# Kernel optimization log

Measured on AMD Instinct MI355X. Metric: run time of the kernel, lower is better.

## Reference

```python
import jax, jax.numpy as jnp
import numpy as np

NUM_USERS = 100000
NUM_ITEMS = 50000
LATENT_DIM = 64
N_EDGES = 600000
BATCH = 4096
N_LAYERS = 4  # K=4, time_split=4, euler -> 4 unit propagation steps


def setup_inputs() -> dict:
    key = jax.random.key(0)
    k1, k2, k3, k4, k5, k6 = jax.random.split(key, 6)
    return {
        "users": jax.random.randint(k1, (BATCH,), 0, NUM_USERS),
        "items": jax.random.randint(k2, (BATCH,), 0, NUM_ITEMS),
        "edge_u": jax.random.randint(k3, (N_EDGES,), 0, NUM_USERS),
        "edge_i": jax.random.randint(k4, (N_EDGES,), 0, NUM_ITEMS),
        "user_emb": 0.1 * jax.random.normal(k5, (NUM_USERS, LATENT_DIM), dtype=jnp.float32),
        "item_emb": 0.1 * jax.random.normal(k6, (NUM_ITEMS, LATENT_DIM), dtype=jnp.float32),
    }


def reference(users, items, edge_u, edge_i, user_emb, item_emb):
    num_users = user_emb.shape[0]
    num_items = item_emb.shape[0]
    N = num_users + num_items

    # symmetric bipartite adjacency as directed edge list
    src = jnp.concatenate([edge_u, edge_i + num_users])
    dst = jnp.concatenate([edge_i + num_users, edge_u])

    # D^{-1/2} A D^{-1/2} edge weights (LightGCN normalization)
    deg = jax.ops.segment_sum(jnp.ones_like(src, dtype=jnp.float32), src, num_segments=N)
    inv_sqrt = jnp.where(deg > 0, jax.lax.rsqrt(jnp.maximum(deg, 1.0)), 0.0)
    w = inv_sqrt[src] * inv_sqrt[dst]  # [2E]

    def spmm(x):  # A_hat @ x via gather-scale-scatter
        return jax.ops.segment_sum(w[:, None] * x[src], dst, num_segments=N)

    x0 = jnp.concatenate([user_emb, item_emb], axis=0)  # [N, d]
    # ODE euler step x + A x, then residual subtraction -> stored emb = A^k x0
    embs = [x0]
    e = x0
    for _ in range(N_LAYERS):
        e = spmm(e)
        embs.append(e)
    light_out = jnp.mean(jnp.stack(embs, axis=1), axis=1)  # [N, d]

    all_users = light_out[:num_users]
    all_items = light_out[num_users:]
    users_emb = all_users[users]
    items_emb = all_items[items]
    gamma = jnp.sum(users_emb * items_emb, axis=1)  # [B]
    return gamma
```

## Files before the change

kernel.cpp:

```cpp
#include <hip/hip_runtime.h>

#define WAVE 64
#define BROWS 256
#define NBKT_MAX 1024
#define CMAX 4
#define SRCMASK 0x3FFFF
#define EPB 2048
#define ENTCAP 4096


__device__ __forceinline__ unsigned short f2bf(float f) {
    unsigned u = __float_as_uint(f);
    u += 0x7FFF + ((u >> 16) & 1);
    return (unsigned short)(u >> 16);
}
__device__ __forceinline__ float bf2f(unsigned short v) {
    return __uint_as_float((unsigned)v << 16);
}
__device__ __forceinline__ void addbf8(float* a, uint4 v) {
    a[0] += __uint_as_float(v.x << 16);
    a[1] += __uint_as_float(v.x & 0xFFFF0000u);
    a[2] += __uint_as_float(v.y << 16);
    a[3] += __uint_as_float(v.y & 0xFFFF0000u);
    a[4] += __uint_as_float(v.z << 16);
    a[5] += __uint_as_float(v.z & 0xFFFF0000u);
    a[6] += __uint_as_float(v.w << 16);
    a[7] += __uint_as_float(v.w & 0xFFFF0000u);
}

__global__ void k_hist(const int* __restrict__ eu, const int* __restrict__ ei,
                       int nE, int nU, int nBkt, int nJg, int* __restrict__ cntBB) {
    __shared__ int h4[4 * NBKT_MAX];
    for (int i = threadIdx.x; i < 4 * nBkt; i += 256) h4[i] = 0;
    __syncthreads();
    int* hw = h4 + (threadIdx.x >> 6) * nBkt;
    const int4* eu4 = (const int4*)eu;
    const int4* ei4 = (const int4*)ei;
    for (int pass = 0; pass < 2; pass++) {
        int i4 = blockIdx.x * 512 + pass * 256 + threadIdx.x;
        int e0 = i4 * 4;
        if (e0 + 3 < nE) {
            int4 u = eu4[i4];
            int4 v = ei4[i4];
            atomicAdd(&hw[u.x >> 8], 1); atomicAdd(&hw[(nU + v.x) >> 8], 1);
            atomicAdd(&hw[u.y >> 8], 1); atomicAdd(&hw[(nU + v.y) >> 8], 1);
            atomicAdd(&hw[u.z >> 8], 1); atomicAdd(&hw[(nU + v.z) >> 8], 1);
            atomicAdd(&hw[u.w >> 8], 1); atomicAdd(&hw[(nU + v.w) >> 8], 1);
        } else if (e0 < nE) {
            for (int e = e0; e < nE; e++) {
                atomicAdd(&hw[eu[e] >> 8], 1);
                atomicAdd(&hw[(nU + ei[e]) >> 8], 1);
            }
        }
    }
    __syncthreads();
    int j = (blockIdx.x & 7) * nJg + (blockIdx.x >> 3);
    int* dst = cntBB + (size_t)j * nBkt;
    for (int i = threadIdx.x; i < nBkt; i += 256)
        dst[i] = h4[i] + h4[nBkt + i] + h4[2 * nBkt + i] + h4[3 * nBkt + i];
}

__global__ void k_scanBkt(const int* __restrict__ cntBB, int* __restrict__ baseBB,
                          int* __restrict__ bktTot, int nBkt, int nJ) {
    __shared__ int s[256];
    int b = blockIdx.x, t = threadIdx.x;
    int C = (nJ + 255) / 256;
    int vals[CMAX];
    int sum = 0;
    for (int k = 0; k < CMAX; k++) {
        if (k >= C) break;
        int j = t * C + k;
        int v = (j < nJ) ? cntBB[(size_t)j * nBkt + b] : 0;
        vals[k] = v; sum += v;
    }
    s[t] = sum;
    __syncthreads();
    for (int o = 1; o < 256; o <<= 1) {
        int x = (t >= o) ? s[t - o] : 0;
        __syncthreads();
        s[t] += x;
        __syncthreads();
    }
    int run = s[t] - sum;
    for (int k = 0; k < CMAX; k++) {
        if (k >= C) break;
        int j = t * C + k;
        if (j < nJ) { baseBB[(size_t)b * nJ + j] = run; run += vals[k]; }
    }
    if (t == 0) bktTot[b] = s[255];
}

__global__ void k_scanTot(const int* __restrict__ bktTot, int* __restrict__ bktBase,
                          int* __restrict__ row_ptr, int nBkt, int N, int total) {
    __shared__ int s[1024];
    int t = threadIdx.x;
    int v = (t < nBkt) ? bktTot[t] : 0;
    s[t] = v;
    __syncthreads();
    for (int o = 1; o < 1024; o <<= 1) {
        int x = (t >= o) ? s[t - o] : 0;
        __syncthreads();
        s[t] += x;
        __syncthreads();
    }
    if (t < nBkt) bktBase[t] = s[t] - v;
    if (t == 0) { bktBase[nBkt] = total; row_ptr[N] = total; }
}

__global__ void k_bin(const int* __restrict__ eu, const int* __restrict__ ei,
                      int nE, int nU, int nBkt, int nJ, int nJg,
                      const int* __restrict__ baseBB, const int* __restrict__ bktBase,
                      int* __restrict__ bins) {
    __shared__ int ent[2 * EPB];
    __shared__ unsigned short ebkt[2 * EPB];
    __shared__ int h2[2 * NBKT_MAX];
    __shared__ int lcur[NBKT_MAX];
    __shared__ int dlt[NBKT_MAX];
    __shared__ int sp[256];
    int t = threadIdx.x;
    int j = (blockIdx.x & 7) * nJg + (blockIdx.x >> 3);
    const bool fullBlk = ((size_t)(blockIdx.x + 1) * EPB <= (size_t)nE);

    if (!fullBlk) {
        for (int i = t; i < nBkt; i += 256)
            lcur[i] = bktBase[i] + baseBB[(size_t)i * nJ + j];
        __syncthreads();
        for (int e = blockIdx.x * EPB + t; e < nE; e += 256) {
            int u = eu[e];
            int v = nU + ei[e];
            int p1 = atomicAdd(&lcur[u >> 8], 1);
            int p2 = atomicAdd(&lcur[v >> 8], 1);
            bins[p1] = ((u & 255) << 18) | v;
            bins[p2] = ((v & 255) << 18) | u;
        }
        return;
    }

    for (int i = t; i < nBkt; i += 256) { h2[i] = 0; h2[NBKT_MAX + i] = 0; }
    __syncthreads();
    int myb[16], mye[16];
    int* hs = h2 + (t >> 7) * NBKT_MAX;
    {
        const int4* eu4 = (const int4*)eu;
        const int4* ei4 = (const int4*)ei;
        #pragma unroll
        for (int pass = 0; pass < 2; pass++) {
            int i4 = blockIdx.x * 512 + pass * 256 + t;
            int4 uu = eu4[i4];
            int4 vv = ei4[i4];
            #pragma unroll
            for (int k = 0; k < 4; k++) {
                int u = (k == 0) ? uu.x : (k == 1) ? uu.y : (k == 2) ? uu.z : uu.w;
                int i2 = (k == 0) ? vv.x : (k == 1) ? vv.y : (k == 2) ? vv.z : vv.w;
                int v = nU + i2;
                int idx = pass * 8 + k * 2;
                myb[idx]     = u >> 8; mye[idx]     = ((u & 255) << 18) | v;
                myb[idx + 1] = v >> 8; mye[idx + 1] = ((v & 255) << 18) | u;
            }
        }
    }
    #pragma unroll
    for (int k = 0; k < 16; k++) atomicAdd(&hs[myb[k]], 1);
    __syncthreads();
    int C = (nBkt + 255) / 256;
    int vals[4];
    int sum = 0;
    for (int k = 0; k < 4; k++) {
        if (k >= C) break;
        int b = t * C + k;
        int v = (b < nBkt) ? (h2[b] + h2[NBKT_MAX + b]) : 0;
        vals[k] = v; sum += v;
    }
    sp[t] = sum;
    __syncthreads();
    for (int o = 1; o < 256; o <<= 1) {
        int x = (t >= o) ? sp[t - o] : 0;
        __syncthreads();
        sp[t] += x;
        __syncthreads();
    }
    int run = sp[t] - sum;
    for (int k = 0; k < 4; k++) {
        if (k >= C) break;
        int b = t * C + k;
        if (b < nBkt) {
            lcur[b] = run;
            int g = bktBase[b] + baseBB[(size_t)b * nJ + j];
            dlt[b] = g - run;
            run += vals[k];
        }
    }
    __syncthreads();
    int n4 = sp[255];
    #pragma unroll
    for (int k = 0; k < 16; k++) {
        int p = atomicAdd(&lcur[myb[k]], 1);
        ent[p] = mye[k];
        ebkt[p] = (unsigned short)myb[k];
    }
    __syncthreads();
    for (int i = t; i < n4; i += 256)
        bins[dlt[ebkt[i]] + i] = ent[i];
}

__global__ void k_csrz(const int* __restrict__ bins, const int* __restrict__ bktBase,
                       int N, int nU,
                       const float* __restrict__ ue, const float* __restrict__ ie,
                       int* __restrict__ row_ptr, int* __restrict__ col,
                       unsigned short* __restrict__ z0) {
    __shared__ int ent[ENTCAP];
    __shared__ int h4[4 * BROWS];
    __shared__ int sc[BROWS];
    __shared__ int cur4[4 * BROWS];
    __shared__ float sInv[BROWS];
    int b = blockIdx.x, t = threadIdx.x, w = t >> 6;
    int base = bktBase[b];
    int n = bktBase[b + 1] - base;
    h4[t] = 0; h4[256 + t] = 0; h4[512 + t] = 0; h4[768 + t] = 0;
    __syncthreads();
    int* hw = h4 + w * BROWS;
    for (int i = t; i < n; i += 256) {
        int p = bins[base + i];
        if (i < ENTCAP) ent[i] = p;
        atomicAdd(&hw[p >> 18], 1);
    }
    __syncthreads();
    int v = h4[t] + h4[256 + t] + h4[512 + t] + h4[768 + t];
    sc[t] = v;
    __syncthreads();
    for (int o = 1; o < 256; o <<= 1) {
        int x = (t >= o) ? sc[t - o] : 0;
        __syncthreads();
        sc[t] += x;
        __syncthreads();
    }
    int excl = sc[t] - v;
    int row = b * BROWS + t;
    if (row < N) row_ptr[row] = base + excl;
    sInv[t] = (v > 0) ? (1.0f / sqrtf((float)v)) : 0.0f;
    cur4[t]       = excl;
    cur4[256 + t] = excl + h4[t];
    cur4[512 + t] = excl + h4[t] + h4[256 + t];
    cur4[768 + t] = excl + h4[t] + h4[256 + t] + h4[512 + t];
    __syncthreads();
    int rf = t & 15, rg = t >> 4;
    for (int pass = 0; pass < 16; pass++) {
        int r = pass * 16 + rg;
        int rr = b * BROWS + r;
        if (rr < N) {
            const float4* src = (rr < nU)
                ? ((const float4*)ue) + (size_t)rr * 16
                : ((const float4*)ie) + (size_t)(rr - nU) * 16;
            float4 val = src[rf];
            float scl = sInv[r];
            ushort4 o;
            o.x = f2bf(val.x * scl);
            o.y = f2bf(val.y * scl);
            o.z = f2bf(val.z * scl);
            o.w = f2bf(val.w * scl);
            ((ushort4*)z0)[(size_t)rr * 16 + rf] = o;
        }
    }
    int* cw = cur4 + w * BROWS;
    for (int i = t; i < n; i += 256) {
        int p = (i < ENTCAP) ? ent[i] : bins[base + i];
        int pos = base + atomicAdd(&cw[p >> 18], 1);
        col[pos] = p & SRCMASK;
    }
}

__global__ void k_spmm(const int* __restrict__ row_ptr, const int* __restrict__ col,
                       const unsigned short* __restrict__ x,
                       unsigned short* __restrict__ y, int N, int nBlkMain,
                       const int* __restrict__ users, const int* __restrict__ items,
                       int B, int nU,
                       const float* __restrict__ ue, const float* __restrict__ ie,
                       float* __restrict__ acc, int mode) {
    int t = threadIdx.x;
    if ((int)blockIdx.x < nBlkMain) {
        int grp = t >> 3, f = t & 7;
        int row = blockIdx.x * 32 + grp;
        if (row >= N) return;
        const uint4* x8 = (const uint4*)x;
        int s = row_ptr[row], e = row_ptr[row + 1];
        float a0[8] = {0,0,0,0,0,0,0,0};
        float a1[8] = {0,0,0,0,0,0,0,0};
        float a2[8] = {0,0,0,0,0,0,0,0};
        float a3[8] = {0,0,0,0,0,0,0,0};
        for (int j = s; j < e; j += 8) {
            #pragma unroll
            for (int k = 0; k < 8; k++) {
                int jj = j + k;
                bool ok = jj < e;
                int c = col[ok ? jj : (e - 1)];
                uint4 v = x8[(size_t)c * 8 + f];
                if (!ok) { v.x = 0; v.y = 0; v.z = 0; v.w = 0; }
                if ((k & 3) == 0) addbf8(a0, v);
                else if ((k & 3) == 1) addbf8(a1, v);
                else if ((k & 3) == 2) addbf8(a2, v);
                else addbf8(a3, v);
            }
        }
        float rdeg = (e > s) ? (1.0f / (float)(e - s)) : 0.0f;
        uint4 o;
        float s0, s1;
        s0 = (a0[0]+a1[0]+a2[0]+a3[0]) * rdeg; s1 = (a0[1]+a1[1]+a2[1]+a3[1]) * rdeg;
        o.x = (unsigned)f2bf(s0) | ((unsigned)f2bf(s1) << 16);
        s0 = (a0[2]+a1[2]+a2[2]+a3[2]) * rdeg; s1 = (a0[3]+a1[3]+a2[3]+a3[3]) * rdeg;
        o.y = (unsigned)f2bf(s0) | ((unsigned)f2bf(s1) << 16);
        s0 = (a0[4]+a1[4]+a2[4]+a3[4]) * rdeg; s1 = (a0[5]+a1[5]+a2[5]+a3[5]) * rdeg;
        o.z = (unsigned)f2bf(s0) | ((unsigned)f2bf(s1) << 16);
        s0 = (a0[6]+a1[6]+a2[6]+a3[6]) * rdeg; s1 = (a0[7]+a1[7]+a2[7]+a3[7]) * rdeg;
        o.w = (unsigned)f2bf(s0) | ((unsigned)f2bf(s1) << 16);
        ((uint4*)y)[(size_t)row * 8 + f] = o;
    } else {
        int grp = t >> 4, f4 = t & 15;
        int b = (blockIdx.x - nBlkMain) * 16 + grp;
        if (b >= 2 * B) return;
        const ushort4* x4 = (const ushort4*)x;
        float4 c;
        if (mode == 0) {
            const float4* x0 = (b < B)
                ? ((const float4*)ue) + (size_t)users[b] * 16
                : ((const float4*)ie) + (size_t)items[b - B] * 16;
            c = x0[f4];
        } else {
            int row = (b < B) ? users[b] : (nU + items[b - B]);
            int deg = row_ptr[row + 1] - row_ptr[row];
            float f = sqrtf((float)deg);
            ushort4 v = x4[(size_t)row * 16 + f4];
            c = ((const float4*)acc)[(size_t)b * 16 + f4];
            c.x += f * bf2f(v.x); c.y += f * bf2f(v.y);
            c.z += f * bf2f(v.z); c.w += f * bf2f(v.w);
        }
        ((float4*)acc)[(size_t)b * 16 + f4] = c;
    }
}

__global__ void k_tail34(const int* __restrict__ row_ptr, const int* __restrict__ col,
                         const unsigned short* __restrict__ z3,
                         const int* __restrict__ users, const int* __restrict__ items,
                         int B, int nU, float* __restrict__ acc) {
    int t = threadIdx.x, grp = t >> 3, f = t & 7;
    int b = blockIdx.x * 32 + grp;
    if (b >= 2 * B) return;
    int row = (b < B) ? users[b] : (nU + items[b - B]);
    int s = row_ptr[row], e = row_ptr[row + 1];
    const uint4* x8 = (const uint4*)z3;
    float4 cA = ((const float4*)acc)[(size_t)b * 16 + 2 * f];
    float4 cB = ((const float4*)acc)[(size_t)b * 16 + 2 * f + 1];
    if (e > s) {
        float fq = sqrtf((float)(e - s));
        float a0[8] = {0,0,0,0,0,0,0,0};
        float a1[8] = {0,0,0,0,0,0,0,0};
        int j = s;
        for (; j + 1 < e; j += 2) {
            uint4 v0 = x8[(size_t)col[j] * 8 + f];
            uint4 v1 = x8[(size_t)col[j + 1] * 8 + f];
            addbf8(a0, v0); addbf8(a1, v1);
        }
        if (j < e) {
            uint4 v0 = x8[(size_t)col[j] * 8 + f];
            addbf8(a0, v0);
        }
        uint4 vs = x8[(size_t)row * 8 + f];
        float self[8] = {0,0,0,0,0,0,0,0};
        addbf8(self, vs);
        float scale = fq / (float)(e - s);
        cA.x += fq * self[0] + scale * (a0[0] + a1[0]);
        cA.y += fq * self[1] + scale * (a0[1] + a1[1]);
        cA.z += fq * self[2] + scale * (a0[2] + a1[2]);
        cA.w += fq * self[3] + scale * (a0[3] + a1[3]);
        cB.x += fq * self[4] + scale * (a0[4] + a1[4]);
        cB.y += fq * self[5] + scale * (a0[5] + a1[5]);
        cB.z += fq * self[6] + scale * (a0[6] + a1[6]);
        cB.w += fq * self[7] + scale * (a0[7] + a1[7]);
    }
    ((float4*)acc)[(size_t)b * 16 + 2 * f]     = cA;
    ((float4*)acc)[(size_t)b * 16 + 2 * f + 1] = cB;
}

__global__ void k_dot(const float* __restrict__ acc, int B, float* __restrict__ out) {
    int b = blockIdx.x * (blockDim.x >> 6) + (threadIdx.x >> 6);
    int lane = threadIdx.x & 63;
    if (b >= B) return;
    float p = acc[(size_t)b * 64 + lane] * acc[(size_t)(b + B) * 64 + lane];
    #pragma unroll
    for (int o = 32; o > 0; o >>= 1) p += __shfl_down(p, o, WAVE);
    if (lane == 0) out[b] = p * (1.0f / 25.0f);
}

extern "C" void kernel_launch(void* const* d_in, const int* in_sizes, int n_in,
                              void* d_out, int out_size, void* d_ws, size_t ws_size,
                              hipStream_t stream) {
    const int*   users = (const int*)d_in[0];
    const int*   items = (const int*)d_in[1];
    const int*   eu    = (const int*)d_in[2];
    const int*   ei    = (const int*)d_in[3];
    const float* ue    = (const float*)d_in[4];
    const float* ie    = (const float*)d_in[5];
    float* out = (float*)d_out;

    const int D  = 64;
    const int B  = in_sizes[0];
    const int nE = in_sizes[2];
    const int nU = in_sizes[4] / D;
    const int nI = in_sizes[5] / D;
    const int N  = nU + nI;
    const int nBkt = (N + BROWS - 1) / BROWS;
    const int total = 2 * nE;

    const int nBlkB = (nE + EPB - 1) / EPB;
    const int nJg   = (nBlkB + 7) / 8;
    const int nJ    = 8 * nJg;

    char* p = (char*)d_ws;
    auto alloc = [&](size_t bytes) -> void* {
        void* r = (void*)p;
        p += (bytes + 255) & ~(size_t)255;
        return r;
    };
    int*   cntBB   = (int*)  alloc((size_t)nJ * nBkt * 4);
    int*   baseBB  = (int*)  alloc((size_t)nBkt * nJ * 4);
    int*   bktTot  = (int*)  alloc((size_t)nBkt * 4);
    int*   bktBase = (int*)  alloc((size_t)(nBkt + 1) * 4);
    int*   bins    = (int*)  alloc((size_t)total * 4);
    int*   col     = (int*)  alloc((size_t)total * 4);
    int*   row_ptr = (int*)  alloc((size_t)(N + 1) * 4);
    unsigned short* za = (unsigned short*)alloc((size_t)N * D * 2);
    unsigned short* zb = (unsigned short*)alloc((size_t)N * D * 2);
    float* acc     = (float*)alloc((size_t)2 * B * D * 4);

    k_hist<<<nJ, 256, 0, stream>>>(eu, ei, nE, nU, nBkt, nJg, cntBB);
    k_scanBkt<<<nBkt, 256, 0, stream>>>(cntBB, baseBB, bktTot, nBkt, nJ);
    k_scanTot<<<1, 1024, 0, stream>>>(bktTot, bktBase, row_ptr, nBkt, N, total);
    k_bin<<<nJ, 256, 0, stream>>>(eu, ei, nE, nU, nBkt, nJ, nJg, baseBB, bktBase, bins);
    k_csrz<<<nBkt, BROWS, 0, stream>>>(bins, bktBase, N, nU, ue, ie, row_ptr, col, za);

    const int nBlkMain = (N + 31) / 32;
    const int nBlkTail = (2 * B + 15) / 16;
    unsigned short* zin = za;
    unsigned short* zout = zb;
    for (int l = 0; l < 3; l++) {
        k_spmm<<<nBlkMain + nBlkTail, 256, 0, stream>>>(
            row_ptr, col, zin, zout, N, nBlkMain,
            users, items, B, nU, ue, ie, acc, (l == 0) ? 0 : 1);
        unsigned short* t = zin; zin = zout; zout = t;
    }

    const int nBlkT34 = (2 * B + 31) / 32;
    k_tail34<<<nBlkT34, 256, 0, stream>>>(row_ptr, col, zin, users, items, B, nU, acc);
    k_dot<<<(B + 3) / 4, 256, 0, stream>>>(acc, B, out);
}
```

Baseline: 210.8 us.

## Fuse CSR build pipeline into one cooperative kernel with grid syncs

Replaces the five separate CSR construction kernels (histogram, per-bucket scan, total scan, binning, CSR+z0 init) with a single cooperative kernel of 512 blocks that steps through the phases separated by grid.sync. The chunk size drops to 1024 edges, and the layer-0 acc initialization moves into the build kernel's otherwise idle blocks, so the first spmm launch no longer needs tail blocks. The goal is to remove launch gaps and kernel-boundary drains between the small phases. In exchange, grid-wide barriers are added, the grid is fixed at 512 blocks that loop over the work, and there are more per-chunk partial counts to scan.

```diff
diff --git a/kernel.cpp b/kernel.cpp
--- a/kernel.cpp
+++ b/kernel.cpp
@@ -1,12 +1,14 @@
 #include <hip/hip_runtime.h>
+#include <hip/hip_cooperative_groups.h>
+
+namespace cg = cooperative_groups;
 
 #define WAVE 64
 #define BROWS 256
-#define NBKT_MAX 1024
-#define CMAX 4
 #define SRCMASK 0x3FFFF
-#define EPB 2048
+#define EPC 1024
 #define ENTCAP 4096
+#define GRID_BUILD 512
 
 
 __device__ __forceinline__ unsigned short f2bf(float f) {
@@ -28,244 +30,267 @@
     a[7] += __uint_as_float(v.w & 0xFFFF0000u);
 }
 
-__global__ void k_hist(const int* __restrict__ eu, const int* __restrict__ ei,
-                       int nE, int nU, int nBkt, int nJg, int* __restrict__ cntBB) {
-    __shared__ int h4[4 * NBKT_MAX];
-    for (int i = threadIdx.x; i < 4 * nBkt; i += 256) h4[i] = 0;
-    __syncthreads();
-    int* hw = h4 + (threadIdx.x >> 6) * nBkt;
-    const int4* eu4 = (const int4*)eu;
-    const int4* ei4 = (const int4*)ei;
-    for (int pass = 0; pass < 2; pass++) {
-        int i4 = blockIdx.x * 512 + pass * 256 + threadIdx.x;
-        int e0 = i4 * 4;
-        if (e0 + 3 < nE) {
-            int4 u = eu4[i4];
-            int4 v = ei4[i4];
-            atomicAdd(&hw[u.x >> 8], 1); atomicAdd(&hw[(nU + v.x) >> 8], 1);
-            atomicAdd(&hw[u.y >> 8], 1); atomicAdd(&hw[(nU + v.y) >> 8], 1);
-            atomicAdd(&hw[u.z >> 8], 1); atomicAdd(&hw[(nU + v.z) >> 8], 1);
-            atomicAdd(&hw[u.w >> 8], 1); atomicAdd(&hw[(nU + v.w) >> 8], 1);
-        } else if (e0 < nE) {
-            for (int e = e0; e < nE; e++) {
-                atomicAdd(&hw[eu[e] >> 8], 1);
-                atomicAdd(&hw[(nU + ei[e]) >> 8], 1);
-            }
-        }
-    }
-    __syncthreads();
-    int j = (blockIdx.x & 7) * nJg + (blockIdx.x >> 3);
-    int* dst = cntBB + (size_t)j * nBkt;
-    for (int i = threadIdx.x; i < nBkt; i += 256)
-        dst[i] = h4[i] + h4[nBkt + i] + h4[2 * nBkt + i] + h4[3 * nBkt + i];
-}
-
-__global__ void k_scanBkt(const int* __restrict__ cntBB, int* __restrict__ baseBB,
-                          int* __restrict__ bktTot, int nBkt, int nJ) {
-    __shared__ int s[256];
-    int b = blockIdx.x, t = threadIdx.x;
-    int C = (nJ + 255) / 256;
-    int vals[CMAX];
-    int sum = 0;
-    for (int k = 0; k < CMAX; k++) {
-        if (k >= C) break;
-        int j = t * C + k;
-        int v = (j < nJ) ? cntBB[(size_t)j * nBkt + b] : 0;
-        vals[k] = v; sum += v;
-    }
-    s[t] = sum;
-    __syncthreads();
-    for (int o = 1; o < 256; o <<= 1) {
-        int x = (t >= o) ? s[t - o] : 0;
+__global__ void k_build(const int* __restrict__ eu, const int* __restrict__ ei,
+                        int nE, int nU, int nBkt, int nChunk,
+                        int* __restrict__ cntBB, int* __restrict__ baseBB,
+                        int* __restrict__ bktTot, int* __restrict__ bktBase,
+                        int* __restrict__ bins, int* __restrict__ row_ptr,
+                        int* __restrict__ col, unsigned short* __restrict__ z0,
+                        const float* __restrict__ ue, const float* __restrict__ ie,
+                        const int* __restrict__ users, const int* __restrict__ items,
+                        int B, float* __restrict__ acc, int N, int total) {
+    cg::grid_group grid = cg::this_grid();
+    __shared__ __align__(16) char smem[30720];
+    int t = threadIdx.x;
+
+    {
+        int* h4 = (int*)smem;
+        for (int c = blockIdx.x; c < nChunk; c += gridDim.x) {
+            for (int i = t; i < 4 * nBkt; i += 256) h4[i] = 0;
+            __syncthreads();
+            int* hw = h4 + (t >> 6) * nBkt;
+            if ((c + 1) * EPC <= nE) {
+                int i4 = c * 256 + t;
+                int4 u = ((const int4*)eu)[i4];
+                int4 v = ((const int4*)ei)[i4];
+                atomicAdd(&hw[u.x >> 8], 1); atomicAdd(&hw[(nU + v.x) >> 8], 1);
+                atomicAdd(&hw[u.y >> 8], 1); atomicAdd(&hw[(nU + v.y) >> 8], 1);
+                atomicAdd(&hw[u.z >> 8], 1); atomicAdd(&hw[(nU + v.z) >> 8], 1);
+                atomicAdd(&hw[u.w >> 8], 1); atomicAdd(&hw[(nU + v.w) >> 8], 1);
+            } else {
+                for (int e = c * EPC + t; e < nE; e += 256) {
+                    atomicAdd(&hw[eu[e] >> 8], 1);
+                    atomicAdd(&hw[(nU + ei[e]) >> 8], 1);
+                }
+            }
+            __syncthreads();
+            int* dst = cntBB + (size_t)c * nBkt;
+            for (int i = t; i < nBkt; i += 256)
+                dst[i] = h4[i] + h4[nBkt + i] + h4[2 * nBkt + i] + h4[3 * nBkt + i];
+            __syncthreads();
+        }
+    }
+    grid.sync();
+
+    {
+        int* sp = (int*)smem;
+        int C = (nChunk + 255) / 256;
+        for (int b = blockIdx.x; b < nBkt; b += gridDim.x) {
+            int vals[4];
+            int sum = 0;
+            for (int k = 0; k < 4; k++) {
+                if (k >= C) break;
+                int j = t * C + k;
+                int v = (j < nChunk) ? cntBB[(size_t)j * nBkt + b] : 0;
+                vals[k] = v; sum += v;
+            }
+            sp[t] = sum;
+            __syncthreads();
+            for (int o = 1; o < 256; o <<= 1) {
+                int x = (t >= o) ? sp[t - o] : 0;
+                __syncthreads();
+                sp[t] += x;
+                __syncthreads();
+            }
+            int run = sp[t] - sum;
+            for (int k = 0; k < 4; k++) {
+                if (k >= C) break;
+                int j = t * C + k;
+                if (j < nChunk) { baseBB[(size_t)b * nChunk + j] = run; run += vals[k]; }
+            }
+            if (t == 0) bktTot[b] = sp[255];
+            __syncthreads();
+        }
+    }
+    grid.sync();
+
+    if (blockIdx.x == 0) {
+        int* sp = (int*)smem;
+        int C = (nBkt + 255) / 256;
+        int vals[4];
+        int sum = 0;
+        for (int k = 0; k < 4; k++) {
+            if (k >= C) break;
+            int i = t * C + k;
+            int v = (i < nBkt) ? bktTot[i] : 0;
+            vals[k] = v; sum += v;
+        }
+        sp[t] = sum;
         __syncthreads();
-        s[t] += x;
-        __syncthreads();
-    }
-    int run = s[t] - sum;
-    for (int k = 0; k < CMAX; k++) {
-        if (k >= C) break;
-        int j = t * C + k;
-        if (j < nJ) { baseBB[(size_t)b * nJ + j] = run; run += vals[k]; }
-    }
-    if (t == 0) bktTot[b] = s[255];
-}
-
-__global__ void k_scanTot(const int* __restrict__ bktTot, int* __restrict__ bktBase,
-                          int* __restrict__ row_ptr, int nBkt, int N, int total) {
-    __shared__ int s[1024];
-    int t = threadIdx.x;
-    int v = (t < nBkt) ? bktTot[t] : 0;
-    s[t] = v;
-    __syncthreads();
-    for (int o = 1; o < 1024; o <<= 1) {
-        int x = (t >= o) ? s[t - o] : 0;
-        __syncthreads();
-        s[t] += x;
-        __syncthreads();
-    }
-    if (t < nBkt) bktBase[t] = s[t] - v;
-    if (t == 0) { bktBase[nBkt] = total; row_ptr[N] = total; }
-}
-
-__global__ void k_bin(const int* __restrict__ eu, const int* __restrict__ ei,
-                      int nE, int nU, int nBkt, int nJ, int nJg,
-                      const int* __restrict__ baseBB, const int* __restrict__ bktBase,
-                      int* __restrict__ bins) {
-    __shared__ int ent[2 * EPB];
-    __shared__ unsigned short ebkt[2 * EPB];
-    __shared__ int h2[2 * NBKT_MAX];
-    __shared__ int lcur[NBKT_MAX];
-    __shared__ int dlt[NBKT_MAX];
-    __shared__ int sp[256];
-    int t = threadIdx.x;
-    int j = (blockIdx.x & 7) * nJg + (blockIdx.x >> 3);
-    const bool fullBlk = ((size_t)(blockIdx.x + 1) * EPB <= (size_t)nE);
-
-    if (!fullBlk) {
-        for (int i = t; i < nBkt; i += 256)
-            lcur[i] = bktBase[i] + baseBB[(size_t)i * nJ + j];
-        __syncthreads();
-        for (int e = blockIdx.x * EPB + t; e < nE; e += 256) {
-            int u = eu[e];
-            int v = nU + ei[e];
-            int p1 = atomicAdd(&lcur[u >> 8], 1);
-            int p2 = atomicAdd(&lcur[v >> 8], 1);
-            bins[p1] = ((u & 255) << 18) | v;
-            bins[p2] = ((v & 255) << 18) | u;
-        }
-        return;
-    }
-
-    for (int i = t; i < nBkt; i += 256) { h2[i] = 0; h2[NBKT_MAX + i] = 0; }
-    __syncthreads();
-    int myb[16], mye[16];
-    int* hs = h2 + (t >> 7) * NBKT_MAX;
+        for (int o = 1; o < 256; o <<= 1) {
+            int x = (t >= o) ? sp[t - o] : 0;
+            __syncthreads();
+            sp[t] += x;
+            __syncthreads();
+        }
+        int run = sp[t] - sum;
+        for (int k = 0; k < 4; k++) {
+            if (k >= C) break;
+            int i = t * C + k;
+            if (i < nBkt) { bktBase[i] = run; run += vals[k]; }
+        }
+        if (t == 0) { bktBase[nBkt] = total; row_ptr[N] = total; }
+    } else {
+        for (int idx = (blockIdx.x - 1) * 256 + t; idx < 2 * B * 16;
+             idx += (gridDim.x - 1) * 256) {
+            int b = idx >> 4, f4 = idx & 15;
+            const float4* x0 = (b < B)
+                ? ((const float4*)ue) + (size_t)users[b] * 16
+                : ((const float4*)ie) + (size_t)items[b - B] * 16;
+            ((float4*)acc)[(size_t)b * 16 + f4] = x0[f4];
+        }
+    }
+    grid.sync();
+
     {
-        const int4* eu4 = (const int4*)eu;
-        const int4* ei4 = (const int4*)ei;
-        #pragma unroll
-        for (int pass = 0; pass < 2; pass++) {
-            int i4 = blockIdx.x * 512 + pass * 256 + t;
-            int4 uu = eu4[i4];
-            int4 vv = ei4[i4];
-            #pragma unroll
-            for (int k = 0; k < 4; k++) {
-                int u = (k == 0) ? uu.x : (k == 1) ? uu.y : (k == 2) ? uu.z : uu.w;
-                int i2 = (k == 0) ? vv.x : (k == 1) ? vv.y : (k == 2) ? vv.z : vv.w;
-                int v = nU + i2;
-                int idx = pass * 8 + k * 2;
-                myb[idx]     = u >> 8; mye[idx]     = ((u & 255) << 18) | v;
-                myb[idx + 1] = v >> 8; mye[idx + 1] = ((v & 255) << 18) | u;
-            }
-        }
-    }
-    #pragma unroll
-    for (int k = 0; k < 16; k++) atomicAdd(&hs[myb[k]], 1);
-    __syncthreads();
-    int C = (nBkt + 255) / 256;
-    int vals[4];
-    int sum = 0;
-    for (int k = 0; k < 4; k++) {
-        if (k >= C) break;
-        int b = t * C + k;
-        int v = (b < nBkt) ? (h2[b] + h2[NBKT_MAX + b]) : 0;
-        vals[k] = v; sum += v;
-    }
-    sp[t] = sum;
-    __syncthreads();
-    for (int o = 1; o < 256; o <<= 1) {
-        int x = (t >= o) ? sp[t - o] : 0;
-        __syncthreads();
-        sp[t] += x;
-        __syncthreads();
-    }
-    int run = sp[t] - sum;
-    for (int k = 0; k < 4; k++) {
-        if (k >= C) break;
-        int b = t * C + k;
-        if (b < nBkt) {
-            lcur[b] = run;
-            int g = bktBase[b] + baseBB[(size_t)b * nJ + j];
-            dlt[b] = g - run;
-            run += vals[k];
-        }
-    }
-    __syncthreads();
-    int n4 = sp[255];
-    #pragma unroll
-    for (int k = 0; k < 16; k++) {
-        int p = atomicAdd(&lcur[myb[k]], 1);
-        ent[p] = mye[k];
-        ebkt[p] = (unsigned short)myb[k];
-    }
-    __syncthreads();
-    for (int i = t; i < n4; i += 256)
-        bins[dlt[ebkt[i]] + i] = ent[i];
-}
-
-__global__ void k_csrz(const int* __restrict__ bins, const int* __restrict__ bktBase,
-                       int N, int nU,
-                       const float* __restrict__ ue, const float* __restrict__ ie,
-                       int* __restrict__ row_ptr, int* __restrict__ col,
-                       unsigned short* __restrict__ z0) {
-    __shared__ int ent[ENTCAP];
-    __shared__ int h4[4 * BROWS];
-    __shared__ int sc[BROWS];
-    __shared__ int cur4[4 * BROWS];
-    __shared__ float sInv[BROWS];
-    int b = blockIdx.x, t = threadIdx.x, w = t >> 6;
-    int base = bktBase[b];
-    int n = bktBase[b + 1] - base;
-    h4[t] = 0; h4[256 + t] = 0; h4[512 + t] = 0; h4[768 + t] = 0;
-    __syncthreads();
-    int* hw = h4 + w * BROWS;
-    for (int i = t; i < n; i += 256) {
-        int p = bins[base + i];
-        if (i < ENTCAP) ent[i] = p;
-        atomicAdd(&hw[p >> 18], 1);
-    }
-    __syncthreads();
-    int v = h4[t] + h4[256 + t] + h4[512 + t] + h4[768 + t];
-    sc[t] = v;
-    __syncthreads();
-    for (int o = 1; o < 256; o <<= 1) {
-        int x = (t >= o) ? sc[t - o] : 0;
-        __syncthreads();
-        sc[t] += x;
-        __syncthreads();
-    }
-    int excl = sc[t] - v;
-    int row = b * BROWS + t;
-    if (row < N) row_ptr[row] = base + excl;
-    sInv[t] = (v > 0) ? (1.0f / sqrtf((float)v)) : 0.0f;
-    cur4[t]       = excl;
-    cur4[256 + t] = excl + h4[t];
-    cur4[512 + t] = excl + h4[t] + h4[256 + t];
-    cur4[768 + t] = excl + h4[t] + h4[256 + t] + h4[512 + t];
-    __syncthreads();
-    int rf = t & 15, rg = t >> 4;
-    for (int pass = 0; pass < 16; pass++) {
-        int r = pass * 16 + rg;
-        int rr = b * BROWS + r;
-        if (rr < N) {
-            const float4* src = (rr < nU)
-                ? ((const float4*)ue) + (size_t)rr * 16
-                : ((const float4*)ie) + (size_t)(rr - nU) * 16;
-            float4 val = src[rf];
-            float scl = sInv[r];
-            ushort4 o;
-            o.x = f2bf(val.x * scl);
-            o.y = f2bf(val.y * scl);
-            o.z = f2bf(val.z * scl);
-            o.w = f2bf(val.w * scl);
-            ((ushort4*)z0)[(size_t)rr * 16 + rf] = o;
-        }
-    }
-    int* cw = cur4 + w * BROWS;
-    for (int i = t; i < n; i += 256) {
-        int p = (i < ENTCAP) ? ent[i] : bins[base + i];
-        int pos = base + atomicAdd(&cw[p >> 18], 1);
-        col[pos] = p & SRCMASK;
+        int* ent            = (int*)smem;
+        unsigned short* ebk = (unsigned short*)(smem + 8192);
+        int* h2             = (int*)(smem + 12288);
+        int* lcur           = (int*)(smem + 20480);
+        int* dlt            = (int*)(smem + 24576);
+        int* sp             = (int*)(smem + 28672);
+        for (int c = blockIdx.x; c < nChunk; c += gridDim.x) {
+            if ((c + 1) * EPC <= nE) {
+                for (int i = t; i < 2 * nBkt; i += 256) h2[i] = 0;
+                __syncthreads();
+                int myb[8], mye[8];
+                {
+                    int i4 = c * 256 + t;
+                    int4 uu = ((const int4*)eu)[i4];
+                    int4 vv = ((const int4*)ei)[i4];
+                    #pragma unroll
+                    for (int k = 0; k < 4; k++) {
+                        int u  = (k == 0) ? uu.x : (k == 1) ? uu.y : (k == 2) ? uu.z : uu.w;
+                        int i2 = (k == 0) ? vv.x : (k == 1) ? vv.y : (k == 2) ? vv.z : vv.w;
+                        int v = nU + i2;
+                        myb[2 * k]     = u >> 8; mye[2 * k]     = ((u & 255) << 18) | v;
+                        myb[2 * k + 1] = v >> 8; mye[2 * k + 1] = ((v & 255) << 18) | u;
+                    }
+                }
+                int* hs = h2 + (t >> 7) * nBkt;
+                #pragma unroll
+                for (int k = 0; k < 8; k++) atomicAdd(&hs[myb[k]], 1);
+                __syncthreads();
+                int C = (nBkt + 255) / 256;
+                int vals[4];
+                int sum = 0;
+                for (int k = 0; k < 4; k++) {
+                    if (k >= C) break;
+                    int b = t * C + k;
+                    int v = (b < nBkt) ? (h2[b] + h2[nBkt + b]) : 0;
+                    vals[k] = v; sum += v;
+                }
+                sp[t] = sum;
+                __syncthreads();
+                for (int o = 1; o < 256; o <<= 1) {
+                    int x = (t >= o) ? sp[t - o] : 0;
+                    __syncthreads();
+                    sp[t] += x;
+                    __syncthreads();
+                }
+                int run = sp[t] - sum;
+                for (int k = 0; k < 4; k++) {
+                    if (k >= C) break;
+                    int b = t * C + k;
+                    if (b < nBkt) {
+                        lcur[b] = run;
+                        dlt[b] = bktBase[b] + baseBB[(size_t)b * nChunk + c] - run;
+                        run += vals[k];
+                    }
+                }
+                __syncthreads();
+                #pragma unroll
+                for (int k = 0; k < 8; k++) {
+                    int p = atomicAdd(&lcur[myb[k]], 1);
+                    ent[p] = mye[k];
+                    ebk[p] = (unsigned short)myb[k];
+                }
+                __syncthreads();
+                int n4 = sp[255];
+                for (int i = t; i < n4; i += 256)
+                    bins[dlt[ebk[i]] + i] = ent[i];
+                __syncthreads();
+            } else {
+                for (int i = t; i < nBkt; i += 256)
+                    lcur[i] = bktBase[i] + baseBB[(size_t)i * nChunk + c];
+                __syncthreads();
+                for (int e = c * EPC + t; e < nE; e += 256) {
+                    int u = eu[e];
+                    int v = nU + ei[e];
+                    int p1 = atomicAdd(&lcur[u >> 8], 1);
+                    int p2 = atomicAdd(&lcur[v >> 8], 1);
+                    bins[p1] = ((u & 255) << 18) | v;
+                    bins[p2] = ((v & 255) << 18) | u;
+                }
+                __syncthreads();
+            }
+        }
+    }
+    grid.sync();
+
+    {
+        int* ent    = (int*)smem;
+        int* h4     = (int*)(smem + 16384);
+        int* cur4   = (int*)(smem + 20480);
+        int* sc     = (int*)(smem + 24576);
+        float* sInv = (float*)(smem + 25600);
+        int w = t >> 6;
+        for (int b = blockIdx.x; b < nBkt; b += gridDim.x) {
+            int base = bktBase[b];
+            int n = bktBase[b + 1] - base;
+            h4[t] = 0; h4[256 + t] = 0; h4[512 + t] = 0; h4[768 + t] = 0;
+            __syncthreads();
+            int* hw = h4 + w * BROWS;
+            for (int i = t; i < n; i += 256) {
+                int p = bins[base + i];
+                if (i < ENTCAP) ent[i] = p;
+                atomicAdd(&hw[p >> 18], 1);
+            }
+            __syncthreads();
+            int v = h4[t] + h4[256 + t] + h4[512 + t] + h4[768 + t];
+            sc[t] = v;
+            __syncthreads();
+            for (int o = 1; o < 256; o <<= 1) {
+                int x = (t >= o) ? sc[t - o] : 0;
+                __syncthreads();
+                sc[t] += x;
+                __syncthreads();
+            }
+            int excl = sc[t] - v;
+            int row = b * BROWS + t;
+            if (row < N) row_ptr[row] = base + excl;
+            sInv[t] = (v > 0) ? (1.0f / sqrtf((float)v)) : 0.0f;
+            cur4[t]       = excl;
+            cur4[256 + t] = excl + h4[t];
+            cur4[512 + t] = excl + h4[t] + h4[256 + t];
+            cur4[768 + t] = excl + h4[t] + h4[256 + t] + h4[512 + t];
+            __syncthreads();
+            int rf = t & 15, rg = t >> 4;
+            for (int pass = 0; pass < 16; pass++) {
+                int r = pass * 16 + rg;
+                int rr = b * BROWS + r;
+                if (rr < N) {
+                    const float4* src = (rr < nU)
+                        ? ((const float4*)ue) + (size_t)rr * 16
+                        : ((const float4*)ie) + (size_t)(rr - nU) * 16;
+                    float4 val = src[rf];
+                    float scl = sInv[r];
+                    ushort4 o;
+                    o.x = f2bf(val.x * scl);
+                    o.y = f2bf(val.y * scl);
+                    o.z = f2bf(val.z * scl);
+                    o.w = f2bf(val.w * scl);
+                    ((ushort4*)z0)[(size_t)rr * 16 + rf] = o;
+                }
+            }
+            int* cw = cur4 + w * BROWS;
+            for (int i = t; i < n; i += 256) {
+                int p = (i < ENTCAP) ? ent[i] : bins[base + i];
+                int pos = base + atomicAdd(&cw[p >> 18], 1);
+                col[pos] = p & SRCMASK;
+            }
+            __syncthreads();
+        }
     }
 }
 
@@ -273,9 +298,7 @@
                        const unsigned short* __restrict__ x,
                        unsigned short* __restrict__ y, int N, int nBlkMain,
                        const int* __restrict__ users, const int* __restrict__ items,
-                       int B, int nU,
-                       const float* __restrict__ ue, const float* __restrict__ ie,
-                       float* __restrict__ acc, int mode) {
+                       int B, int nU, float* __restrict__ acc, int mode) {
     int t = threadIdx.x;
     if ((int)blockIdx.x < nBlkMain) {
         int grp = t >> 3, f = t & 7;
@@ -314,25 +337,18 @@
         o.w = (unsigned)f2bf(s0) | ((unsigned)f2bf(s1) << 16);
         ((uint4*)y)[(size_t)row * 8 + f] = o;
     } else {
+        if (mode == 0) return;
         int grp = t >> 4, f4 = t & 15;
         int b = (blockIdx.x - nBlkMain) * 16 + grp;
         if (b >= 2 * B) return;
         const ushort4* x4 = (const ushort4*)x;
-        float4 c;
-        if (mode == 0) {
-            const float4* x0 = (b < B)
-                ? ((const float4*)ue) + (size_t)users[b] * 16
-                : ((const float4*)ie) + (size_t)items[b - B] * 16;
-            c = x0[f4];
-        } else {
-            int row = (b < B) ? users[b] : (nU + items[b - B]);
-            int deg = row_ptr[row + 1] - row_ptr[row];
-            float f = sqrtf((float)deg);
-            ushort4 v = x4[(size_t)row * 16 + f4];
-            c = ((const float4*)acc)[(size_t)b * 16 + f4];
-            c.x += f * bf2f(v.x); c.y += f * bf2f(v.y);
-            c.z += f * bf2f(v.z); c.w += f * bf2f(v.w);
-        }
+        int row = (b < B) ? users[b] : (nU + items[b - B]);
+        int deg = row_ptr[row + 1] - row_ptr[row];
+        float f = sqrtf((float)deg);
+        ushort4 v = x4[(size_t)row * 16 + f4];
+        float4 c = ((const float4*)acc)[(size_t)b * 16 + f4];
+        c.x += f * bf2f(v.x); c.y += f * bf2f(v.y);
+        c.z += f * bf2f(v.z); c.w += f * bf2f(v.w);
         ((float4*)acc)[(size_t)b * 16 + f4] = c;
     }
 }
@@ -402,17 +418,14 @@
     float* out = (float*)d_out;
 
     const int D  = 64;
-    const int B  = in_sizes[0];
-    const int nE = in_sizes[2];
-    const int nU = in_sizes[4] / D;
+    int B  = in_sizes[0];
+    int nE = in_sizes[2];
+    int nU = in_sizes[4] / D;
     const int nI = in_sizes[5] / D;
-    const int N  = nU + nI;
-    const int nBkt = (N + BROWS - 1) / BROWS;
-    const int total = 2 * nE;
-
-    const int nBlkB = (nE + EPB - 1) / EPB;
-    const int nJg   = (nBlkB + 7) / 8;
-    const int nJ    = 8 * nJg;
+    int N  = nU + nI;
+    int nBkt = (N + BROWS - 1) / BROWS;
+    int total = 2 * nE;
+    int nChunk = (nE + EPC - 1) / EPC;
 
     char* p = (char*)d_ws;
     auto alloc = [&](size_t bytes) -> void* {
@@ -420,8 +433,8 @@
         p += (bytes + 255) & ~(size_t)255;
         return r;
     };
-    int*   cntBB   = (int*)  alloc((size_t)nJ * nBkt * 4);
-    int*   baseBB  = (int*)  alloc((size_t)nBkt * nJ * 4);
+    int*   cntBB   = (int*)  alloc((size_t)nChunk * nBkt * 4);
+    int*   baseBB  = (int*)  alloc((size_t)nBkt * nChunk * 4);
     int*   bktTot  = (int*)  alloc((size_t)nBkt * 4);
     int*   bktBase = (int*)  alloc((size_t)(nBkt + 1) * 4);
     int*   bins    = (int*)  alloc((size_t)total * 4);
@@ -431,20 +444,29 @@
     unsigned short* zb = (unsigned short*)alloc((size_t)N * D * 2);
     float* acc     = (float*)alloc((size_t)2 * B * D * 4);
 
-    k_hist<<<nJ, 256, 0, stream>>>(eu, ei, nE, nU, nBkt, nJg, cntBB);
-    k_scanBkt<<<nBkt, 256, 0, stream>>>(cntBB, baseBB, bktTot, nBkt, nJ);
-    k_scanTot<<<1, 1024, 0, stream>>>(bktTot, bktBase, row_ptr, nBkt, N, total);
-    k_bin<<<nJ, 256, 0, stream>>>(eu, ei, nE, nU, nBkt, nJ, nJg, baseBB, bktBase, bins);
-    k_csrz<<<nBkt, BROWS, 0, stream>>>(bins, bktBase, N, nU, ue, ie, row_ptr, col, za);
+    {
+        const int* eu_ = eu; const int* ei_ = ei;
+        const float* ue_ = ue; const float* ie_ = ie;
+        const int* users_ = users; const int* items_ = items;
+        void* args[] = {
+            (void*)&eu_, (void*)&ei_, (void*)&nE, (void*)&nU, (void*)&nBkt,
+            (void*)&nChunk, (void*)&cntBB, (void*)&baseBB, (void*)&bktTot,
+            (void*)&bktBase, (void*)&bins, (void*)&row_ptr, (void*)&col,
+            (void*)&za, (void*)&ue_, (void*)&ie_, (void*)&users_, (void*)&items_,
+            (void*)&B, (void*)&acc, (void*)&N, (void*)&total };
+        hipLaunchCooperativeKernel((void*)k_build, dim3(GRID_BUILD), dim3(256),
+                                   args, 0, stream);
+    }
 
     const int nBlkMain = (N + 31) / 32;
     const int nBlkTail = (2 * B + 15) / 16;
     unsigned short* zin = za;
     unsigned short* zout = zb;
     for (int l = 0; l < 3; l++) {
-        k_spmm<<<nBlkMain + nBlkTail, 256, 0, stream>>>(
-            row_ptr, col, zin, zout, N, nBlkMain,
-            users, items, B, nU, ue, ie, acc, (l == 0) ? 0 : 1);
+        int mode = (l == 0) ? 0 : 1;
+        int nBlk = nBlkMain + ((l == 0) ? 0 : nBlkTail);
+        k_spmm<<<nBlk, 256, 0, stream>>>(row_ptr, col, zin, zout, N, nBlkMain,
+                                         users, items, B, nU, acc, mode);
         unsigned short* t = zin; zin = zout; zout = t;
     }
 
```

Result: slower. 466.0 us (+121.0%).
